# Performance work log

Measured on AMD Instinct MI355X. Metric: run time of the kernel, lower is better.

## Reference

```python
import jax, jax.numpy as jnp
import numpy as np

def setup_inputs() -> dict:
    key = jax.random.key(0)
    ks = jax.random.split(key, 8)
    E, D_IN, D_OUT = 250000, 256, 256
    NUM_CAMS, NUM_POINTS = 500, 100000
    return {
        "edge_features": jax.random.normal(ks[0], (E, D_IN), dtype=jnp.float32),
        "cam_indices": jax.random.randint(ks[1], (E,), 0, NUM_CAMS, dtype=jnp.int64 if jax.config.jax_enable_x64 else jnp.int32),
        "point_indices": jax.random.randint(ks[2], (E,), 0, NUM_POINTS, dtype=jnp.int64 if jax.config.jax_enable_x64 else jnp.int32),
        "num_cams": NUM_CAMS,
        "num_points": NUM_POINTS,
        "W_cam": jax.random.normal(ks[3], (D_OUT, D_IN), dtype=jnp.float32) / np.sqrt(D_IN),
        "W_point": jax.random.normal(ks[4], (D_OUT, D_IN), dtype=jnp.float32) / np.sqrt(D_IN),
        "W_attn": jax.random.normal(ks[5], (1, 2 * D_OUT), dtype=jnp.float32) / np.sqrt(2 * D_OUT),
        "W_final": jax.random.normal(ks[6], (D_OUT, 2 * D_OUT), dtype=jnp.float32) / np.sqrt(2 * D_OUT),
        "b_final": jax.random.normal(ks[7], (D_OUT,), dtype=jnp.float32) * 0.01,
    }

def reference(edge_features, cam_indices, point_indices, num_cams, num_points,
              W_cam, W_point, W_attn, W_final, b_final):
    # scatter-add aggregation per camera / per point node
    cam_agg = jax.ops.segment_sum(edge_features, cam_indices, num_segments=num_cams)      # [C, d_in]
    point_agg = jax.ops.segment_sum(edge_features, point_indices, num_segments=num_points)  # [P, d_in]
    # node projections (torch Linear: y = x @ W.T)
    h_cam = cam_agg @ W_cam.T        # [C, d_out]
    h_point = point_agg @ W_point.T  # [P, d_out]
    # gather back per edge and concat
    concat = jnp.concatenate([h_cam[cam_indices], h_point[point_indices]], axis=1)  # [E, 2*d_out]
    # attention score with GLOBAL softmax over all edges (dim=0)
    e = concat @ W_attn.T                       # [E, 1]
    attn = jax.nn.softmax(e, axis=0)            # [E, 1]
    new_features = (concat @ W_final.T + b_final) * attn  # [E, d_out]
    return jax.nn.relu(new_features)
```

## Files before the change

kernel.cpp:

```cpp
#include <hip/hip_runtime.h>
#include <hip/hip_bf16.h>
#include <math.h>

#define D 256
#define NCAM 500
#define NPT 100000
#define SCAN_NB ((NPT + 1023) / 1024)

__global__ void hist_kernel(const int* __restrict__ ci, const int* __restrict__ pi,
                            int* __restrict__ cnt_pt, int* __restrict__ cnt_cam, int E) {
    int i = blockIdx.x * 256 + threadIdx.x;
    if (i < E) {
        atomicAdd(&cnt_pt[pi[i]], 1);
        atomicAdd(&cnt_cam[ci[i]], 1);
    }
}

__global__ __launch_bounds__(1024) void scan_partA(const int* __restrict__ cnt_pt,
                                                   int* __restrict__ blk_sum) {
    __shared__ int lds[1024];
    int t = threadIdx.x;
    int i = blockIdx.x * 1024 + t;
    lds[t] = (i < NPT) ? cnt_pt[i] : 0;
    __syncthreads();
    for (int s = 512; s > 0; s >>= 1) {
        if (t < s) lds[t] += lds[t + s];
        __syncthreads();
    }
    if (t == 0) blk_sum[blockIdx.x] = lds[0];
}

__global__ __launch_bounds__(512) void scan_partB(const int* __restrict__ blk_sum,
                                                  int* __restrict__ blk_base,
                                                  int* __restrict__ off_pt,
                                                  const int* __restrict__ cnt_cam,
                                                  int* __restrict__ off_cam,
                                                  int* __restrict__ cur_cam) {
    __shared__ int lds[512];
    int t = threadIdx.x;
    lds[t] = (t < SCAN_NB) ? blk_sum[t] : 0;
    __syncthreads();
    for (int off = 1; off < 512; off <<= 1) {
        int v = (t >= off) ? lds[t - off] : 0;
        __syncthreads();
        lds[t] += v;
        __syncthreads();
    }
    if (t < SCAN_NB) blk_base[t] = (t == 0) ? 0 : lds[t - 1];
    if (t == SCAN_NB) off_pt[NPT] = lds[SCAN_NB - 1];
    __syncthreads();
    lds[t] = (t < NCAM) ? cnt_cam[t] : 0;
    __syncthreads();
    for (int off = 1; off < 512; off <<= 1) {
        int v = (t >= off) ? lds[t - off] : 0;
        __syncthreads();
        lds[t] += v;
        __syncthreads();
    }
    if (t < NCAM) {
        int ex = (t == 0) ? 0 : lds[t - 1];
        off_cam[t] = ex;
        cur_cam[t] = ex;
    }
    if (t == NCAM) off_cam[NCAM] = lds[NCAM - 1];
}

__global__ __launch_bounds__(1024) void scan_partC(const int* __restrict__ cnt_pt,
                                                   const int* __restrict__ blk_base,
                                                   int* __restrict__ off_pt,
                                                   int* __restrict__ cur_pt) {
    __shared__ int lds[1024];
    int t = threadIdx.x;
    int i = blockIdx.x * 1024 + t;
    lds[t] = (i < NPT) ? cnt_pt[i] : 0;
    __syncthreads();
    for (int off = 1; off < 1024; off <<= 1) {
        int v = (t >= off) ? lds[t - off] : 0;
        __syncthreads();
        lds[t] += v;
        __syncthreads();
    }
    if (i < NPT) {
        int ex = blk_base[blockIdx.x] + ((t == 0) ? 0 : lds[t - 1]);
        off_pt[i] = ex;
        cur_pt[i] = ex;
    }
}

__global__ void bucket_kernel(const int* __restrict__ ci, const int* __restrict__ pi,
                              int* __restrict__ cur_pt, int* __restrict__ cur_cam,
                              int* __restrict__ order_pt, int* __restrict__ order_cam,
                              int E) {
    int i = blockIdx.x * 256 + threadIdx.x;
    if (i < E) {
        int pos = atomicAdd(&cur_pt[pi[i]], 1);
        order_pt[pos] = i;
        int pos2 = atomicAdd(&cur_cam[ci[i]], 1);
        order_cam[pos2] = i;
    }
}

__global__ void pt_agg_kernel(const float* __restrict__ ef,
                              const int* __restrict__ order_pt,
                              const int* __restrict__ off_pt,
                              const float* __restrict__ vpt,
                              float* __restrict__ pt_agg,
                              float* __restrict__ apt) {
    int wave = threadIdx.x >> 6;
    int lane = threadIdx.x & 63;
    int p = blockIdx.x * 4 + wave;
    if (p >= NPT) return;
    int j0 = off_pt[p], j1 = off_pt[p + 1];
    float4 acc = make_float4(0.f, 0.f, 0.f, 0.f);
    for (int j = j0; j < j1; j++) {
        int e = order_pt[j];
        float4 v = *(const float4*)(ef + (size_t)e * D + lane * 4);
        acc.x += v.x; acc.y += v.y; acc.z += v.z; acc.w += v.w;
    }
    *(float4*)(pt_agg + (size_t)p * D + lane * 4) = acc;
    float4 vv = *(const float4*)(vpt + lane * 4);
    float d = acc.x * vv.x + acc.y * vv.y + acc.z * vv.z + acc.w * vv.w;
    for (int off = 32; off > 0; off >>= 1) d += __shfl_down(d, off);
    if (lane == 0) apt[p] = d;
}

__global__ void cam_agg_kernel(const float* __restrict__ ef,
                               const int* __restrict__ order_cam,
                               const int* __restrict__ off_cam,
                               float* __restrict__ cam_agg) {
    int c = blockIdx.x;
    int q = blockIdx.y;
    int t = threadIdx.x;
    int j0 = off_cam[c], j1 = off_cam[c + 1];
    float acc = 0.f;
    for (int j = j0 + q; j < j1; j += 8) {
        int e = order_cam[j];
        acc += ef[(size_t)e * D + t];
    }
    atomicAdd(&cam_agg[(size_t)c * D + t], acc);
}

__global__ void combine_weights(const float* __restrict__ Wcam,
                                const float* __restrict__ Wpt,
                                const float* __restrict__ Wattn,
                                const float* __restrict__ Wfin,
                                float* __restrict__ CcamT,
                                float* __restrict__ Cpt,
                                float* __restrict__ vcam,
                                float* __restrict__ vpt) {
    int b = blockIdx.x;
    int i = threadIdx.x;
    if (b < 256) {
        int o = b;
        float acc = 0.f;
        for (int j = 0; j < 256; j++) acc += Wfin[o * 512 + j] * Wcam[j * 256 + i];
        CcamT[i * 256 + o] = acc;
    } else if (b < 512) {
        int o = b - 256;
        float acc = 0.f;
        for (int j = 0; j < 256; j++) acc += Wfin[o * 512 + 256 + j] * Wpt[j * 256 + i];
        Cpt[o * 256 + i] = acc;
    } else if (b == 512) {
        float acc = 0.f;
        for (int j = 0; j < 256; j++) acc += Wattn[j] * Wcam[j * 256 + i];
        vcam[i] = acc;
    } else {
        float acc = 0.f;
        for (int j = 0; j < 256; j++) acc += Wattn[256 + j] * Wpt[j * 256 + i];
        vpt[i] = acc;
    }
}

__global__ void cam_proj(const float* __restrict__ cam_agg,
                         const float* __restrict__ CcamT,
                         const float* __restrict__ vcam,
                         float* __restrict__ gcam,
                         float* __restrict__ acam) {
    __shared__ float row[256];
    __shared__ float red[256];
    int c = blockIdx.x;
    int t = threadIdx.x;
    row[t] = cam_agg[(size_t)c * 256 + t];
    __syncthreads();
    float acc = 0.f;
    for (int i = 0; i < 256; i++) acc += row[i] * CcamT[i * 256 + t];
    gcam[(size_t)c * 256 + t] = acc;
    red[t] = row[t] * vcam[t];
    __syncthreads();
    for (int s = 128; s > 0; s >>= 1) {
        if (t < s) red[t] += red[t + s];
        __syncthreads();
    }
    if (t == 0) acam[c] = red[0];
}

#define BM 64
#define BN 64
#define BK 32
__global__ __launch_bounds__(256) void gemm_pt(const float* __restrict__ A,
                                               const float* __restrict__ Bmat,
                                               float* __restrict__ Cout, int M) {
    __shared__ float As[BK][BM + 4];
    __shared__ float Bs[BK][BN + 4];
    int m0 = blockIdx.x * BM;
    int n0 = blockIdx.y * BN;
    int tid = threadIdx.x;
    int arow = tid >> 2;
    int acol = (tid & 3) * 8;
    int tm = (tid >> 4) << 2;
    int tn = (tid & 15) << 2;
    float acc[4][4] = {};
    for (int k0 = 0; k0 < 256; k0 += BK) {
        const float* aptr = A + (size_t)(m0 + arow) * 256 + k0 + acol;
        float4 av0 = *(const float4*)aptr;
        float4 av1 = *(const float4*)(aptr + 4);
        const float* bptr = Bmat + (size_t)(n0 + arow) * 256 + k0 + acol;
        float4 bv0 = *(const float4*)bptr;
        float4 bv1 = *(const float4*)(bptr + 4);
        As[acol + 0][arow] = av0.x; As[acol + 1][arow] = av0.y;
        As[acol + 2][arow] = av0.z; As[acol + 3][arow] = av0.w;
        As[acol + 4][arow] = av1.x; As[acol + 5][arow] = av1.y;
        As[acol + 6][arow] = av1.z; As[acol + 7][arow] = av1.w;
        Bs[acol + 0][arow] = bv0.x; Bs[acol + 1][arow] = bv0.y;
        Bs[acol + 2][arow] = bv0.z; Bs[acol + 3][arow] = bv0.w;
        Bs[acol + 4][arow] = bv1.x; Bs[acol + 5][arow] = bv1.y;
        Bs[acol + 6][arow] = bv1.z; Bs[acol + 7][arow] = bv1.w;
        __syncthreads();
#pragma unroll
        for (int k = 0; k < BK; k++) {
            float4 a = *(const float4*)&As[k][tm];
            float4 b = *(const float4*)&Bs[k][tn];
            acc[0][0] += a.x * b.x; acc[0][1] += a.x * b.y; acc[0][2] += a.x * b.z; acc[0][3] += a.x * b.w;
            acc[1][0] += a.y * b.x; acc[1][1] += a.y * b.y; acc[1][2] += a.y * b.z; acc[1][3] += a.y * b.w;
            acc[2][0] += a.z * b.x; acc[2][1] += a.z * b.y; acc[2][2] += a.z * b.z; acc[2][3] += a.z * b.w;
            acc[3][0] += a.w * b.x; acc[3][1] += a.w * b.y; acc[3][2] += a.w * b.z; acc[3][3] += a.w * b.w;
        }
        __syncthreads();
    }
#pragma unroll
    for (int i = 0; i < 4; i++) {
        int m = m0 + tm + i;
        if (m < M) {
            float4 v = make_float4(acc[i][0], acc[i][1], acc[i][2], acc[i][3]);
            *(float4*)&Cout[(size_t)m * 256 + n0 + tn] = v;
        }
    }
}

__device__ __forceinline__ unsigned float_key(float f) {
    unsigned b = __float_as_uint(f);
    return (b & 0x80000000u) ? ~b : (b | 0x80000000u);
}
__device__ __forceinline__ float key_float(unsigned k) {
    return __uint_as_float((k & 0x80000000u) ? (k & 0x7FFFFFFFu) : ~k);
}

__global__ void e_max_kernel(const int* __restrict__ ci, const int* __restrict__ pi,
                             const float* __restrict__ acam, const float* __restrict__ apt,
                             float* __restrict__ ebuf, unsigned* __restrict__ maxkey, int E) {
    int i = blockIdx.x * 256 + threadIdx.x;
    float e = -INFINITY;
    if (i < E) {
        e = acam[ci[i]] + apt[pi[i]];
        ebuf[i] = e;
    }
    __shared__ float red[256];
    int t = threadIdx.x;
    red[t] = e;
    __syncthreads();
    for (int s = 128; s > 0; s >>= 1) {
        if (t < s) red[t] = fmaxf(red[t], red[t + s]);
        __syncthreads();
    }
    if (t == 0) atomicMax(maxkey, float_key(red[0]));
}

__global__ void sumexp_kernel(float* __restrict__ ebuf,
                              const unsigned* __restrict__ maxkey,
                              float* __restrict__ sumexp, int E) {
    int i = blockIdx.x * 256 + threadIdx.x;
    float mx = key_float(*maxkey);
    float p = 0.f;
    if (i < E) {
        p = expf(ebuf[i] - mx);
        ebuf[i] = p;
    }
    __shared__ float red[256];
    int t = threadIdx.x;
    red[t] = p;
    __syncthreads();
    for (int s = 128; s > 0; s >>= 1) {
        if (t < s) red[t] += red[t + s];
        __syncthreads();
    }
    if (t == 0) atomicAdd(sumexp, red[0]);
}

__global__ void out_kernel(const int* __restrict__ ci, const int* __restrict__ pi,
                           const float* __restrict__ gcam, const float* __restrict__ gpt,
                           const float* __restrict__ bfin, const float* __restrict__ ebuf,
                           const float* __restrict__ sumexp, float* __restrict__ out, int E) {
    int e = blockIdx.x;
    int t = threadIdx.x;
    float scale = ebuf[e] / (*sumexp);
    int c = ci[e];
    int p = pi[e];
    float v = (gcam[(size_t)c * 256 + t] + gpt[(size_t)p * 256 + t] + bfin[t]) * scale;
    out[(size_t)e * 256 + t] = fmaxf(v, 0.f);
}

extern "C" void kernel_launch(void* const* d_in, const int* in_sizes, int n_in,
                              void* d_out, int out_size, void* d_ws, size_t ws_size,
                              hipStream_t stream) {
    const float* ef    = (const float*)d_in[0];
    const int*   ci    = (const int*)d_in[1];
    const int*   pi    = (const int*)d_in[2];
    const float* Wcam  = (const float*)d_in[5];
    const float* Wpt   = (const float*)d_in[6];
    const float* Wattn = (const float*)d_in[7];
    const float* Wfin  = (const float*)d_in[8];
    const float* bfin  = (const float*)d_in[9];
    float* out = (float*)d_out;
    int E = in_sizes[0] / D;

    float* ws = (float*)d_ws;
    float* cam_agg = ws;
    float* pt_agg  = cam_agg + (size_t)NCAM * D;
    float* CcamT   = pt_agg + (size_t)NPT * D;
    float* Cpt     = CcamT + 65536;
    float* vcam    = Cpt + 65536;
    float* vpt     = vcam + 256;
    float* gcam    = vpt + 256;
    float* acam    = gcam + (size_t)NCAM * D;
    float* gpt     = acam + 512;
    float* apt     = gpt + (size_t)NPT * D;
    float* ebuf    = apt + NPT;
    unsigned* maxkey = (unsigned*)(ebuf + E);
    float* sumexp  = (float*)(maxkey + 1);

    int* ib        = (int*)gpt;
    int* cnt_pt    = ib;
    int* cnt_cam   = cnt_pt + NPT;
    int* off_pt    = cnt_cam + NCAM;
    int* off_cam   = off_pt + NPT + 1;
    int* cur_pt    = off_cam + NCAM + 1;
    int* cur_cam   = cur_pt + NPT;
    int* order_pt  = cur_cam + NCAM;
    int* order_cam = order_pt + E;
    int* blk_sum   = order_cam + E;
    int* blk_base  = blk_sum + SCAN_NB;

    hipMemsetAsync(cam_agg, 0, (size_t)NCAM * D * sizeof(float), stream);
    hipMemsetAsync(maxkey, 0, 2 * sizeof(unsigned), stream);
    hipMemsetAsync(cnt_pt, 0, (size_t)(NPT + NCAM) * sizeof(int), stream);

    int eb = (E + 255) / 256;
    hist_kernel<<<eb, 256, 0, stream>>>(ci, pi, cnt_pt, cnt_cam, E);
    combine_weights<<<514, 256, 0, stream>>>(Wcam, Wpt, Wattn, Wfin, CcamT, Cpt, vcam, vpt);
    scan_partA<<<SCAN_NB, 1024, 0, stream>>>(cnt_pt, blk_sum);
    scan_partB<<<1, 512, 0, stream>>>(blk_sum, blk_base, off_pt, cnt_cam, off_cam, cur_cam);
    scan_partC<<<SCAN_NB, 1024, 0, stream>>>(cnt_pt, blk_base, off_pt, cur_pt);
    bucket_kernel<<<eb, 256, 0, stream>>>(ci, pi, cur_pt, cur_cam, order_pt, order_cam, E);
    pt_agg_kernel<<<(NPT + 3) / 4, 256, 0, stream>>>(ef, order_pt, off_pt, vpt, pt_agg, apt);
    cam_agg_kernel<<<dim3(NCAM, 8), 256, 0, stream>>>(ef, order_cam, off_cam, cam_agg);
    cam_proj<<<NCAM, 256, 0, stream>>>(cam_agg, CcamT, vcam, gcam, acam);
    dim3 g4((NPT + BM - 1) / BM, 256 / BN);
    gemm_pt<<<g4, 256, 0, stream>>>(pt_agg, Cpt, gpt, NPT);
    e_max_kernel<<<eb, 256, 0, stream>>>(ci, pi, acam, apt, ebuf, maxkey, E);
    sumexp_kernel<<<eb, 256, 0, stream>>>(ebuf, maxkey, sumexp, E);
    out_kernel<<<E, 256, 0, stream>>>(ci, pi, gcam, gpt, bfin, ebuf, sumexp, out, E);
}
```

Baseline: 1.122 ms.

## Use split-bf16 MFMA for point GEMM and vectorize grid-stride output kernel

The point projection GEMM moves from a scalar FP32 LDS-tiled kernel to MFMA bf16 instructions. Each FP32 operand is split into high and low bf16 parts, and three MFMA products are summed to keep near-FP32 accuracy. The pt_agg and combine_weights kernels now write these split bf16 buffers instead of FP32. Separately, the output kernel changes from one 256-thread block per edge to a grid-stride loop with one wave per edge and float4 loads and stores, which cuts launch and block overhead. The MFMA kernel reads operands directly from global memory without LDS staging, so it may depend on cache hits.

```diff
diff --git a/kernel.cpp b/kernel.cpp
--- a/kernel.cpp
+++ b/kernel.cpp
@@ -6,6 +6,18 @@
 #define NCAM 500
 #define NPT 100000
 #define SCAN_NB ((NPT + 1023) / 1024)
+
+typedef __attribute__((ext_vector_type(8))) short bf16x8;
+typedef __attribute__((ext_vector_type(4))) float f32x4;
+
+__device__ __forceinline__ unsigned short f2bf(float f) {
+    unsigned u = __float_as_uint(f);
+    u += 0x7FFFu + ((u >> 16) & 1u);
+    return (unsigned short)(u >> 16);
+}
+__device__ __forceinline__ float bf2f(unsigned short h) {
+    return __uint_as_float((unsigned)h << 16);
+}
 
 __global__ void hist_kernel(const int* __restrict__ ci, const int* __restrict__ pi,
                             int* __restrict__ cnt_pt, int* __restrict__ cnt_cam, int E) {
@@ -104,7 +116,8 @@
                               const int* __restrict__ order_pt,
                               const int* __restrict__ off_pt,
                               const float* __restrict__ vpt,
-                              float* __restrict__ pt_agg,
+                              unsigned short* __restrict__ Ahi,
+                              unsigned short* __restrict__ Alo,
                               float* __restrict__ apt) {
     int wave = threadIdx.x >> 6;
     int lane = threadIdx.x & 63;
@@ -117,7 +130,13 @@
         float4 v = *(const float4*)(ef + (size_t)e * D + lane * 4);
         acc.x += v.x; acc.y += v.y; acc.z += v.z; acc.w += v.w;
     }
-    *(float4*)(pt_agg + (size_t)p * D + lane * 4) = acc;
+    ushort4 h, l;
+    h.x = f2bf(acc.x); l.x = f2bf(acc.x - bf2f(h.x));
+    h.y = f2bf(acc.y); l.y = f2bf(acc.y - bf2f(h.y));
+    h.z = f2bf(acc.z); l.z = f2bf(acc.z - bf2f(h.z));
+    h.w = f2bf(acc.w); l.w = f2bf(acc.w - bf2f(h.w));
+    *(ushort4*)(Ahi + (size_t)p * D + lane * 4) = h;
+    *(ushort4*)(Alo + (size_t)p * D + lane * 4) = l;
     float4 vv = *(const float4*)(vpt + lane * 4);
     float d = acc.x * vv.x + acc.y * vv.y + acc.z * vv.z + acc.w * vv.w;
     for (int off = 32; off > 0; off >>= 1) d += __shfl_down(d, off);
@@ -145,7 +164,8 @@
                                 const float* __restrict__ Wattn,
                                 const float* __restrict__ Wfin,
                                 float* __restrict__ CcamT,
-                                float* __restrict__ Cpt,
+                                unsigned short* __restrict__ Bhi,
+                                unsigned short* __restrict__ Blo,
                                 float* __restrict__ vcam,
                                 float* __restrict__ vpt) {
     int b = blockIdx.x;
@@ -159,7 +179,9 @@
         int o = b - 256;
         float acc = 0.f;
         for (int j = 0; j < 256; j++) acc += Wfin[o * 512 + 256 + j] * Wpt[j * 256 + i];
-        Cpt[o * 256 + i] = acc;
+        unsigned short h = f2bf(acc);
+        Bhi[o * 256 + i] = h;
+        Blo[o * 256 + i] = f2bf(acc - bf2f(h));
     } else if (b == 512) {
         float acc = 0.f;
         for (int j = 0; j < 256; j++) acc += Wattn[j] * Wcam[j * 256 + i];
@@ -194,55 +216,56 @@
     if (t == 0) acam[c] = red[0];
 }
 
-#define BM 64
-#define BN 64
-#define BK 32
-__global__ __launch_bounds__(256) void gemm_pt(const float* __restrict__ A,
-                                               const float* __restrict__ Bmat,
-                                               float* __restrict__ Cout, int M) {
-    __shared__ float As[BK][BM + 4];
-    __shared__ float Bs[BK][BN + 4];
-    int m0 = blockIdx.x * BM;
-    int n0 = blockIdx.y * BN;
-    int tid = threadIdx.x;
-    int arow = tid >> 2;
-    int acol = (tid & 3) * 8;
-    int tm = (tid >> 4) << 2;
-    int tn = (tid & 15) << 2;
-    float acc[4][4] = {};
-    for (int k0 = 0; k0 < 256; k0 += BK) {
-        const float* aptr = A + (size_t)(m0 + arow) * 256 + k0 + acol;
-        float4 av0 = *(const float4*)aptr;
-        float4 av1 = *(const float4*)(aptr + 4);
-        const float* bptr = Bmat + (size_t)(n0 + arow) * 256 + k0 + acol;
-        float4 bv0 = *(const float4*)bptr;
-        float4 bv1 = *(const float4*)(bptr + 4);
-        As[acol + 0][arow] = av0.x; As[acol + 1][arow] = av0.y;
-        As[acol + 2][arow] = av0.z; As[acol + 3][arow] = av0.w;
-        As[acol + 4][arow] = av1.x; As[acol + 5][arow] = av1.y;
-        As[acol + 6][arow] = av1.z; As[acol + 7][arow] = av1.w;
-        Bs[acol + 0][arow] = bv0.x; Bs[acol + 1][arow] = bv0.y;
-        Bs[acol + 2][arow] = bv0.z; Bs[acol + 3][arow] = bv0.w;
-        Bs[acol + 4][arow] = bv1.x; Bs[acol + 5][arow] = bv1.y;
-        Bs[acol + 6][arow] = bv1.z; Bs[acol + 7][arow] = bv1.w;
-        __syncthreads();
-#pragma unroll
-        for (int k = 0; k < BK; k++) {
-            float4 a = *(const float4*)&As[k][tm];
-            float4 b = *(const float4*)&Bs[k][tn];
-            acc[0][0] += a.x * b.x; acc[0][1] += a.x * b.y; acc[0][2] += a.x * b.z; acc[0][3] += a.x * b.w;
-            acc[1][0] += a.y * b.x; acc[1][1] += a.y * b.y; acc[1][2] += a.y * b.z; acc[1][3] += a.y * b.w;
-            acc[2][0] += a.z * b.x; acc[2][1] += a.z * b.y; acc[2][2] += a.z * b.z; acc[2][3] += a.z * b.w;
-            acc[3][0] += a.w * b.x; acc[3][1] += a.w * b.y; acc[3][2] += a.w * b.z; acc[3][3] += a.w * b.w;
+__global__ __launch_bounds__(256) void gemm_mfma(const unsigned short* __restrict__ Ahi,
+                                                 const unsigned short* __restrict__ Alo,
+                                                 const unsigned short* __restrict__ Bhi,
+                                                 const unsigned short* __restrict__ Blo,
+                                                 float* __restrict__ Cout, int M) {
+    int wave = threadIdx.x >> 6;
+    int lane = threadIdx.x & 63;
+    int m0 = blockIdx.x * 64;
+    int n0 = wave * 64;
+    int fr = lane & 15;
+    int kg = (lane >> 4) * 8;
+    f32x4 acc[4][4] = {};
+    size_t ar[4];
+#pragma unroll
+    for (int f = 0; f < 4; f++) {
+        int row = m0 + f * 16 + fr;
+        if (row >= M) row = M - 1;
+        ar[f] = (size_t)row * 256 + kg;
+    }
+    size_t brow = (size_t)(n0 + fr) * 256 + kg;
+    for (int k0 = 0; k0 < 256; k0 += 32) {
+        bf16x8 ah[4], al[4], bh[4], bl[4];
+#pragma unroll
+        for (int f = 0; f < 4; f++) {
+            ah[f] = *(const bf16x8*)(Ahi + ar[f] + k0);
+            al[f] = *(const bf16x8*)(Alo + ar[f] + k0);
+            bh[f] = *(const bf16x8*)(Bhi + brow + (size_t)f * 16 * 256 + k0);
+            bl[f] = *(const bf16x8*)(Blo + brow + (size_t)f * 16 * 256 + k0);
         }
-        __syncthreads();
-    }
-#pragma unroll
-    for (int i = 0; i < 4; i++) {
-        int m = m0 + tm + i;
-        if (m < M) {
-            float4 v = make_float4(acc[i][0], acc[i][1], acc[i][2], acc[i][3]);
-            *(float4*)&Cout[(size_t)m * 256 + n0 + tn] = v;
+#pragma unroll
+        for (int mf = 0; mf < 4; mf++) {
+#pragma unroll
+            for (int nf = 0; nf < 4; nf++) {
+                acc[mf][nf] = __builtin_amdgcn_mfma_f32_16x16x32_bf16(ah[mf], bh[nf], acc[mf][nf], 0, 0, 0);
+                acc[mf][nf] = __builtin_amdgcn_mfma_f32_16x16x32_bf16(ah[mf], bl[nf], acc[mf][nf], 0, 0, 0);
+                acc[mf][nf] = __builtin_amdgcn_mfma_f32_16x16x32_bf16(al[mf], bh[nf], acc[mf][nf], 0, 0, 0);
+            }
+        }
+    }
+    int rbase = (lane >> 4) * 4;
+#pragma unroll
+    for (int mf = 0; mf < 4; mf++) {
+#pragma unroll
+        for (int r = 0; r < 4; r++) {
+            int row = m0 + mf * 16 + rbase + r;
+            if (row < M) {
+#pragma unroll
+                for (int nf = 0; nf < 4; nf++)
+                    Cout[(size_t)row * 256 + n0 + nf * 16 + fr] = acc[mf][nf][r];
+            }
         }
     }
 }
@@ -296,17 +319,28 @@
     if (t == 0) atomicAdd(sumexp, red[0]);
 }
 
-__global__ void out_kernel(const int* __restrict__ ci, const int* __restrict__ pi,
+__global__ __launch_bounds__(256) void out_kernel(const int* __restrict__ ci, const int* __restrict__ pi,
                            const float* __restrict__ gcam, const float* __restrict__ gpt,
                            const float* __restrict__ bfin, const float* __restrict__ ebuf,
                            const float* __restrict__ sumexp, float* __restrict__ out, int E) {
-    int e = blockIdx.x;
-    int t = threadIdx.x;
-    float scale = ebuf[e] / (*sumexp);
-    int c = ci[e];
-    int p = pi[e];
-    float v = (gcam[(size_t)c * 256 + t] + gpt[(size_t)p * 256 + t] + bfin[t]) * scale;
-    out[(size_t)e * 256 + t] = fmaxf(v, 0.f);
+    int lane = threadIdx.x & 63;
+    int wid = (blockIdx.x * 256 + threadIdx.x) >> 6;
+    int nw = (gridDim.x * 256) >> 6;
+    float inv = 1.0f / (*sumexp);
+    float4 bb = *(const float4*)(bfin + lane * 4);
+    for (int e = wid; e < E; e += nw) {
+        float scale = ebuf[e] * inv;
+        int c = ci[e];
+        int p = pi[e];
+        float4 gc = *(const float4*)(gcam + (size_t)c * 256 + lane * 4);
+        float4 gp = *(const float4*)(gpt + (size_t)p * 256 + lane * 4);
+        float4 v;
+        v.x = fmaxf((gc.x + gp.x + bb.x) * scale, 0.f);
+        v.y = fmaxf((gc.y + gp.y + bb.y) * scale, 0.f);
+        v.z = fmaxf((gc.z + gp.z + bb.z) * scale, 0.f);
+        v.w = fmaxf((gc.w + gp.w + bb.w) * scale, 0.f);
+        *(float4*)(out + (size_t)e * 256 + lane * 4) = v;
+    }
 }
 
 extern "C" void kernel_launch(void* const* d_in, const int* in_sizes, int n_in,
@@ -325,10 +359,14 @@
 
     float* ws = (float*)d_ws;
     float* cam_agg = ws;
-    float* pt_agg  = cam_agg + (size_t)NCAM * D;
-    float* CcamT   = pt_agg + (size_t)NPT * D;
-    float* Cpt     = CcamT + 65536;
-    float* vcam    = Cpt + 65536;
+    float* aregion = cam_agg + (size_t)NCAM * D;
+    unsigned short* Ahi = (unsigned short*)aregion;
+    unsigned short* Alo = Ahi + (size_t)NPT * D;
+    float* CcamT   = aregion + (size_t)NPT * D;
+    float* bregion = CcamT + 65536;
+    unsigned short* Bhi = (unsigned short*)bregion;
+    unsigned short* Blo = Bhi + 65536;
+    float* vcam    = bregion + 65536;
     float* vpt     = vcam + 256;
     float* gcam    = vpt + 256;
     float* acam    = gcam + (size_t)NCAM * D;
@@ -356,17 +394,16 @@
 
     int eb = (E + 255) / 256;
     hist_kernel<<<eb, 256, 0, stream>>>(ci, pi, cnt_pt, cnt_cam, E);
-    combine_weights<<<514, 256, 0, stream>>>(Wcam, Wpt, Wattn, Wfin, CcamT, Cpt, vcam, vpt);
+    combine_weights<<<514, 256, 0, stream>>>(Wcam, Wpt, Wattn, Wfin, CcamT, Bhi, Blo, vcam, vpt);
     scan_partA<<<SCAN_NB, 1024, 0, stream>>>(cnt_pt, blk_sum);
     scan_partB<<<1, 512, 0, stream>>>(blk_sum, blk_base, off_pt, cnt_cam, off_cam, cur_cam);
     scan_partC<<<SCAN_NB, 1024, 0, stream>>>(cnt_pt, blk_base, off_pt, cur_pt);
     bucket_kernel<<<eb, 256, 0, stream>>>(ci, pi, cur_pt, cur_cam, order_pt, order_cam, E);
-    pt_agg_kernel<<<(NPT + 3) / 4, 256, 0, stream>>>(ef, order_pt, off_pt, vpt, pt_agg, apt);
+    pt_agg_kernel<<<(NPT + 3) / 4, 256, 0, stream>>>(ef, order_pt, off_pt, vpt, Ahi, Alo, apt);
     cam_agg_kernel<<<dim3(NCAM, 8), 256, 0, stream>>>(ef, order_cam, off_cam, cam_agg);
     cam_proj<<<NCAM, 256, 0, stream>>>(cam_agg, CcamT, vcam, gcam, acam);
-    dim3 g4((NPT + BM - 1) / BM, 256 / BN);
-    gemm_pt<<<g4, 256, 0, stream>>>(pt_agg, Cpt, gpt, NPT);
+    gemm_mfma<<<(NPT + 63) / 64, 256, 0, stream>>>(Ahi, Alo, Bhi, Blo, gpt, NPT);
     e_max_kernel<<<eb, 256, 0, stream>>>(ci, pi, acam, apt, ebuf, maxkey, E);
     sumexp_kernel<<<eb, 256, 0, stream>>>(ebuf, maxkey, sumexp, E);
-    out_kernel<<<E, 256, 0, stream>>>(ci, pi, gcam, gpt, bfin, ebuf, sumexp, out, E);
-}
+    out_kernel<<<2048, 256, 0, stream>>>(ci, pi, gcam, gpt, bfin, ebuf, sumexp, out, E);
+}
```

Result: faster. 983.2 us (-12.4%).
